# Performance work log

Measured on AMD Instinct MI355X. Metric: run time of the kernel, lower is better.

Reference implementation:

```python
import jax, jax.numpy as jnp
import numpy as np

N_FZ, N_KEZ, N_TINT, N_ALPHA = 60, 20, 30, 200
NORB, NTIMES = 2000, 1000


def setup_inputs() -> dict:
    key = jax.random.key(0)
    k1, k2, k3, k4 = jax.random.split(key, 4)
    # log-spaced coordinate axes (as built in __init__ from fZs / alphas)
    log_fZs = jnp.linspace(-11.0, -9.0, N_FZ, dtype=jnp.float32)
    log_alphas = jnp.linspace(-2.0, 0.0, N_ALPHA, dtype=jnp.float32)
    alphas = 10.0 ** log_alphas
    kEZs = jnp.linspace(0.5, 10.0, N_KEZ, dtype=jnp.float32)  # sorted for searchsorted
    # grid already in stored layout (n_fZ, n_kEZ, n_tint, n_alpha)
    grid = 20.0 + 5.0 * jax.random.uniform(k1, (N_FZ, N_KEZ, N_TINT, N_ALPHA), dtype=jnp.float32)
    # angular separations, mostly inside [alphas[0], alphas[-1]] with some outside
    alpha = 10.0 ** jax.random.uniform(k2, (NORB, NTIMES), minval=-2.2, maxval=0.1, dtype=jnp.float32)
    dMag = 20.0 + 5.0 * jax.random.uniform(k3, (NORB, NTIMES), dtype=jnp.float32)
    fZ_vals = 10.0 ** jax.random.uniform(k4, (NTIMES,), minval=-11.0, maxval=-9.0, dtype=jnp.float32)
    kEZ_val = jnp.asarray(3.0, dtype=jnp.float32)
    return dict(alpha=alpha, dMag=dMag, fZ_vals=fZ_vals, kEZ_val=kEZ_val,
                grid=grid, kEZs=kEZs, alphas=alphas, log_fZs=log_fZs, log_alphas=log_alphas)


def reference(alpha, dMag, fZ_vals, kEZ_val, grid, kEZs, alphas, log_fZs, log_alphas):
    """Faithful translation of dMag0Grid._pdet_alpha_dMag.

    alpha, dMag : (norb, ntimes); fZ_vals : (ntimes,); kEZ_val : scalar.
    grid : (n_fZ, n_kEZ, n_tint, n_alpha).  Returns pdet : (ntimes, n_tint).
    """
    n_fZ = grid.shape[0]
    n_alpha = grid.shape[-1]
    inv_log_fZ_step = 1.0 / (log_fZs[1] - log_fZs[0])
    inv_log_alpha_step = 1.0 / (log_alphas[1] - log_alphas[0])

    geom_mask = (alpha >= alphas[0]) & (alpha <= alphas[-1])  # (norb, ntimes)

    # log-binned fZ index, per time
    fZ_ind = (jnp.log10(fZ_vals) - log_fZs[0]) * inv_log_fZ_step
    fZ0 = jnp.clip(jnp.floor(fZ_ind).astype(jnp.int32) + 1, 0, n_fZ - 2)  # (ntimes,)

    # log-binned alpha index, per (orbit, time)
    a_ind = (jnp.log10(alpha) - log_alphas[0]) * inv_log_alpha_step
    a0 = jnp.clip(a_ind.astype(jnp.int32), 0, n_alpha - 1)  # (norb, ntimes)
    dalpha = (a_ind - a0).astype(grid.dtype)

    kEZ_ind = jnp.searchsorted(kEZs, kEZ_val, side='right') - 1  # scalar

    # dynamic_slice clamps start so the size-2 window stays in bounds
    a0s = jnp.minimum(a0, n_alpha - 2)
    fZb = jnp.broadcast_to(fZ0[None, :], a0.shape)  # (norb, ntimes)

    sub = grid[:, kEZ_ind]          # (n_fZ, n_tint, n_alpha)
    g0 = sub[fZb, :, a0s]           # (norb, ntimes, n_tint) gather
    g1 = sub[fZb, :, a0s + 1]
    dim = g0 + dalpha[..., None] * (g1 - g0)  # linear interp in log-alpha

    det_mask = geom_mask[..., None] & jnp.signbit(dMag[..., None] - dim)
    pdet = det_mask.mean(axis=0)    # (ntimes, n_tint)
    return pdet
```

## Files before the change

kernel.cpp:

```cpp
#include <hip/hip_runtime.h>
#include <math.h>

#define N_FZ    60
#define N_KEZ   20
#define N_TINT  30
#define N_ALPHA 200
#define NORB    2000
#define NTIMES  1000
#define BLOCK   1024
#define PAIR_LD 34
#define N_ROWS  199

__global__ __launch_bounds__(256) void prep_kernel(
    const float* __restrict__ alpha,
    const float* __restrict__ dMag,
    const float* __restrict__ alphas,
    const float* __restrict__ log_alphas,
    float2* __restrict__ xd)
{
    __shared__ float2 tile[32][33];

    const float la0    = log_alphas[0];
    const float inv_la = 1.0f / (log_alphas[1] - la0);
    const float alo    = alphas[0];
    const float ahi    = alphas[N_ALPHA - 1];

    const int t0 = blockIdx.x * 32;
    const int o0 = blockIdx.y * 32;
    const int tx = threadIdx.x, ty = threadIdx.y;

    #pragma unroll
    for (int r = 0; r < 4; ++r) {
        int orb = o0 + ty + 8 * r;
        int t   = t0 + tx;
        float2 v = make_float2(0.0f, __builtin_inff());
        if (orb < NORB && t < NTIMES) {
            float a  = alpha[(size_t)orb * NTIMES + t];
            float dm = dMag [(size_t)orb * NTIMES + t];
            bool geom = (a >= alo) && (a <= ahi);
            float x = (log10f(a) - la0) * inv_la;
            float xc = fminf(fmaxf(x, 0.0f), 198.9999f);
            v = make_float2(xc, geom ? dm : __builtin_inff());
        }
        tile[ty + 8 * r][tx] = v;
    }
    __syncthreads();
    #pragma unroll
    for (int r = 0; r < 4; ++r) {
        int tt  = ty + 8 * r;
        int t   = t0 + tt;
        int orb = o0 + tx;
        if (orb < NORB && t < NTIMES)
            xd[(size_t)t * NORB + orb] = tile[tx][tt];
    }
}

__global__ __launch_bounds__(BLOCK) void pdet6_kernel(
    const float2* __restrict__ xd,
    const float* __restrict__ fZ_vals,
    const float* __restrict__ kEZ_val,
    const float* __restrict__ grid,
    const float* __restrict__ kEZs,
    const float* __restrict__ log_fZs,
    float* __restrict__ out)
{
    __shared__ __align__(16) float2 gsT[N_ROWS * PAIR_LD];
    __shared__ int wsum[16][N_TINT];

    const int t   = blockIdx.x;
    const int tid = threadIdx.x;

    const float lf0    = log_fZs[0];
    const float lfstep = log_fZs[1] - lf0;
    double fZ_ind = (log10((double)fZ_vals[t]) - (double)lf0) * (1.0 / (double)lfstep);
    int fZ0 = (int)floor(fZ_ind) + 1;
    fZ0 = min(max(fZ0, 0), N_FZ - 2);

    const float kv = kEZ_val[0];
    int kidx = -1;
    #pragma unroll
    for (int i = 0; i < N_KEZ; ++i) kidx += (kEZs[i] <= kv) ? 1 : 0;
    if (kidx < 0) kidx += N_KEZ;

    const float* src = grid + ((size_t)fZ0 * N_KEZ + kidx) * (N_TINT * N_ALPHA);
    for (int m = tid; m < N_TINT * 256; m += BLOCK) {
        int k = m >> 8;
        int a = m & 255;
        if (a < N_ROWS) {
            const float* p = src + (size_t)k * N_ALPHA + a;
            float g0 = p[0];
            float g1 = p[1];
            gsT[a * PAIR_LD + k] = make_float2(g0, g1 - g0);
        }
    }
    __syncthreads();

    const int lane = tid & 63;
    const int w    = tid >> 6;
    const int s    = lane >> 4;
    const int h    = lane & 15;
    const int hh   = (h < 15) ? h : 14;

    const float2* row = xd + (size_t)t * NORB;

    int cnt_e = 0, cnt_o = 0;
    #pragma unroll 8
    for (int i = 0; i < 31; ++i) {
        int q = w + 16 * i;
        float2 v = row[4 * q + s];
        unsigned a0 = (unsigned)v.x;
        float dal = __builtin_amdgcn_fractf(v.x);
        float4 P = *reinterpret_cast<const float4*>(&gsT[a0 * PAIR_LD + 2 * hh]);
        cnt_e += (v.y < fmaf(dal, P.y, P.x)) ? 1 : 0;
        cnt_o += (v.y < fmaf(dal, P.w, P.z)) ? 1 : 0;
    }
    if (w < 4) {
        int q = 496 + w;
        float2 v = row[4 * q + s];
        unsigned a0 = (unsigned)v.x;
        float dal = __builtin_amdgcn_fractf(v.x);
        float4 P = *reinterpret_cast<const float4*>(&gsT[a0 * PAIR_LD + 2 * hh]);
        cnt_e += (v.y < fmaf(dal, P.y, P.x)) ? 1 : 0;
        cnt_o += (v.y < fmaf(dal, P.w, P.z)) ? 1 : 0;
    }

    cnt_e += __shfl_xor(cnt_e, 16, 64);
    cnt_e += __shfl_xor(cnt_e, 32, 64);
    cnt_o += __shfl_xor(cnt_o, 16, 64);
    cnt_o += __shfl_xor(cnt_o, 32, 64);
    if (lane < 15) {
        wsum[w][2 * lane]     = cnt_e;
        wsum[w][2 * lane + 1] = cnt_o;
    }
    __syncthreads();

    if (tid < N_TINT) {
        int tot = 0;
        #pragma unroll
        for (int w2 = 0; w2 < 16; ++w2) tot += wsum[w2][tid];
        out[(size_t)t * N_TINT + tid] = (float)tot * (1.0f / NORB);
    }
}

__global__ __launch_bounds__(256) void pdet_kernel(
    const float* __restrict__ alpha, const float* __restrict__ dMag,
    const float* __restrict__ fZ_vals, const float* __restrict__ kEZ_val,
    const float* __restrict__ grid, const float* __restrict__ kEZs,
    const float* __restrict__ alphas, const float* __restrict__ log_fZs,
    const float* __restrict__ log_alphas, float* __restrict__ out)
{
    __shared__ float2 pairs[N_TINT * (N_ALPHA + 1)];
    __shared__ int    wsum[4][N_TINT];

    const int t   = blockIdx.x;
    const int tid = threadIdx.x;

    const float la0    = log_alphas[0];
    const float inv_la = 1.0f / (log_alphas[1] - la0);
    const float alo    = alphas[0];
    const float ahi    = alphas[N_ALPHA - 1];

    const float lf0    = log_fZs[0];
    const float lfstep = log_fZs[1] - lf0;
    double fZ_ind = (log10((double)fZ_vals[t]) - (double)lf0) * (1.0 / (double)lfstep);
    int fZ0 = (int)floor(fZ_ind) + 1;
    fZ0 = min(max(fZ0, 0), N_FZ - 2);

    const float kv = kEZ_val[0];
    int kidx = -1;
    #pragma unroll
    for (int i = 0; i < N_KEZ; ++i) kidx += (kEZs[i] <= kv) ? 1 : 0;
    if (kidx < 0) kidx += N_KEZ;

    const float* src = grid + ((size_t)fZ0 * N_KEZ + kidx) * (N_TINT * N_ALPHA);
    for (int j = tid; j < N_TINT * N_ALPHA; j += 256) {
        int k = j / N_ALPHA;
        int a = j - k * N_ALPHA;
        float g0 = src[j];
        float g1 = (a < N_ALPHA - 1) ? src[j + 1] : g0;
        pairs[k * (N_ALPHA + 1) + a] = make_float2(g0, g1);
    }
    __syncthreads();

    int cnt[N_TINT];
    #pragma unroll
    for (int k = 0; k < N_TINT; ++k) cnt[k] = 0;

    for (int orb = tid; orb < NORB; orb += 256) {
        float a  = alpha[(size_t)orb * NTIMES + t];
        float dm = dMag [(size_t)orb * NTIMES + t];
        bool geom = (a >= alo) && (a <= ahi);
        float a_ind = (log10f(a) - la0) * inv_la;
        int a0 = (int)a_ind;
        a0 = min(max(a0, 0), N_ALPHA - 1);
        float dal = a_ind - (float)a0;
        int a0s = min(a0, N_ALPHA - 2);
        if (!geom) dm = __builtin_inff();

        #pragma unroll
        for (int k = 0; k < N_TINT; ++k) {
            float2 p = pairs[k * (N_ALPHA + 1) + a0s];
            float dim = p.x + dal * (p.y - p.x);
            cnt[k] += (dm < dim) ? 1 : 0;
        }
    }

    const int lane = tid & 63;
    const int wid  = tid >> 6;
    #pragma unroll
    for (int k = 0; k < N_TINT; ++k) {
        int c = cnt[k];
        c += __shfl_xor(c, 32, 64);
        c += __shfl_xor(c, 16, 64);
        c += __shfl_xor(c,  8, 64);
        c += __shfl_xor(c,  4, 64);
        c += __shfl_xor(c,  2, 64);
        c += __shfl_xor(c,  1, 64);
        if (lane == 0) wsum[wid][k] = c;
    }
    __syncthreads();

    if (tid < N_TINT) {
        int tot = wsum[0][tid] + wsum[1][tid] + wsum[2][tid] + wsum[3][tid];
        out[(size_t)t * N_TINT + tid] = (float)tot / (float)NORB;
    }
}

extern "C" void kernel_launch(void* const* d_in, const int* in_sizes, int n_in,
                              void* d_out, int out_size, void* d_ws, size_t ws_size,
                              hipStream_t stream) {
    const float* alpha      = (const float*)d_in[0];
    const float* dMag       = (const float*)d_in[1];
    const float* fZ_vals    = (const float*)d_in[2];
    const float* kEZ_val    = (const float*)d_in[3];
    const float* grid       = (const float*)d_in[4];
    const float* kEZs       = (const float*)d_in[5];
    const float* alphas     = (const float*)d_in[6];
    const float* log_fZs    = (const float*)d_in[7];
    const float* log_alphas = (const float*)d_in[8];
    float* out = (float*)d_out;

    const size_t need = (size_t)NTIMES * NORB * sizeof(float2);
    if (ws_size >= need) {
        dim3 gb((NTIMES + 31) / 32, (NORB + 31) / 32);
        dim3 tb(32, 8);
        prep_kernel<<<gb, tb, 0, stream>>>(alpha, dMag, alphas, log_alphas,
                                           (float2*)d_ws);
        pdet6_kernel<<<NTIMES, BLOCK, 0, stream>>>(
            (const float2*)d_ws, fZ_vals, kEZ_val, grid, kEZs, log_fZs, out);
    } else {
        pdet_kernel<<<NTIMES, 256, 0, stream>>>(
            alpha, dMag, fZ_vals, kEZ_val, grid, kEZs, alphas, log_fZs,
            log_alphas, out);
    }
}
```

Before: 119.9 us.

## Store interpolation table as fp16 pairs and process four t_int values per lane

The shared-memory table of (g0, g1-g0) pairs is packed as half2 instead of float2, which halves the table size. Each lane now reads a uint4 covering four integration-time entries and handles two orbit records per float4 load, so the work is split into 8 lanes per record instead of 16. This aims to cut LDS traffic and the number of instructions in the count loop. The cost is fp16 rounding of grid values around 20-25, which can flip detection comparisons close to the threshold and may drift from the reference.

```diff
diff --git a/kernel.cpp b/kernel.cpp
--- a/kernel.cpp
+++ b/kernel.cpp
@@ -1,4 +1,5 @@
 #include <hip/hip_runtime.h>
+#include <hip/hip_fp16.h>
 #include <math.h>
 
 #define N_FZ    60
@@ -8,7 +9,7 @@
 #define NORB    2000
 #define NTIMES  1000
 #define BLOCK   1024
-#define PAIR_LD 34
+#define ROW_U32 36
 #define N_ROWS  199
 
 __global__ __launch_bounds__(256) void prep_kernel(
@@ -55,7 +56,7 @@
     }
 }
 
-__global__ __launch_bounds__(BLOCK) void pdet6_kernel(
+__global__ __launch_bounds__(BLOCK) void pdet8_kernel(
     const float2* __restrict__ xd,
     const float* __restrict__ fZ_vals,
     const float* __restrict__ kEZ_val,
@@ -64,8 +65,8 @@
     const float* __restrict__ log_fZs,
     float* __restrict__ out)
 {
-    __shared__ __align__(16) float2 gsT[N_ROWS * PAIR_LD];
-    __shared__ int wsum[16][N_TINT];
+    __shared__ __align__(16) unsigned gsT[N_ROWS * ROW_U32];
+    __shared__ int wsum[16][32];
 
     const int t   = blockIdx.x;
     const int tid = threadIdx.x;
@@ -83,54 +84,75 @@
     if (kidx < 0) kidx += N_KEZ;
 
     const float* src = grid + ((size_t)fZ0 * N_KEZ + kidx) * (N_TINT * N_ALPHA);
-    for (int m = tid; m < N_TINT * 256; m += BLOCK) {
+    for (int m = tid; m < 32 * 256; m += BLOCK) {
         int k = m >> 8;
         int a = m & 255;
         if (a < N_ROWS) {
-            const float* p = src + (size_t)k * N_ALPHA + a;
-            float g0 = p[0];
-            float g1 = p[1];
-            gsT[a * PAIR_LD + k] = make_float2(g0, g1 - g0);
+            unsigned val = 0u;
+            if (k < N_TINT) {
+                const float* p = src + (size_t)k * N_ALPHA + a;
+                float g0 = p[0];
+                float g1 = p[1];
+                __half2 h2 = __halves2half2(__float2half(g0), __float2half(g1 - g0));
+                val = *reinterpret_cast<unsigned*>(&h2);
+            }
+            gsT[a * ROW_U32 + k] = val;
         }
     }
     __syncthreads();
 
     const int lane = tid & 63;
     const int w    = tid >> 6;
-    const int s    = lane >> 4;
-    const int h    = lane & 15;
-    const int hh   = (h < 15) ? h : 14;
-
-    const float2* row = xd + (size_t)t * NORB;
-
-    int cnt_e = 0, cnt_o = 0;
-    #pragma unroll 8
-    for (int i = 0; i < 31; ++i) {
-        int q = w + 16 * i;
-        float2 v = row[4 * q + s];
-        unsigned a0 = (unsigned)v.x;
-        float dal = __builtin_amdgcn_fractf(v.x);
-        float4 P = *reinterpret_cast<const float4*>(&gsT[a0 * PAIR_LD + 2 * hh]);
-        cnt_e += (v.y < fmaf(dal, P.y, P.x)) ? 1 : 0;
-        cnt_o += (v.y < fmaf(dal, P.w, P.z)) ? 1 : 0;
-    }
-    if (w < 4) {
-        int q = 496 + w;
-        float2 v = row[4 * q + s];
-        unsigned a0 = (unsigned)v.x;
-        float dal = __builtin_amdgcn_fractf(v.x);
-        float4 P = *reinterpret_cast<const float4*>(&gsT[a0 * PAIR_LD + 2 * hh]);
-        cnt_e += (v.y < fmaf(dal, P.y, P.x)) ? 1 : 0;
-        cnt_o += (v.y < fmaf(dal, P.w, P.z)) ? 1 : 0;
-    }
-
-    cnt_e += __shfl_xor(cnt_e, 16, 64);
-    cnt_e += __shfl_xor(cnt_e, 32, 64);
-    cnt_o += __shfl_xor(cnt_o, 16, 64);
-    cnt_o += __shfl_xor(cnt_o, 32, 64);
-    if (lane < 15) {
-        wsum[w][2 * lane]     = cnt_e;
-        wsum[w][2 * lane + 1] = cnt_o;
+    const int s    = lane >> 3;
+    const int h    = lane & 7;
+    const int hoff = 4 * h;
+
+    int c0 = 0, c1 = 0, c2 = 0, c3 = 0;
+
+    const float4* rp = reinterpret_cast<const float4*>(xd + (size_t)t * NORB)
+                     + 8 * w + s;
+
+    #define EVALREC(XC, DM)                                                      \
+    do {                                                                         \
+        unsigned a0_ = (unsigned)(XC);                                           \
+        float dal_ = __builtin_amdgcn_fractf(XC);                                \
+        uint4 U_ = *reinterpret_cast<const uint4*>(&gsT[a0_ * ROW_U32 + hoff]);  \
+        __half2 p0_ = *reinterpret_cast<const __half2*>(&U_.x);                  \
+        __half2 p1_ = *reinterpret_cast<const __half2*>(&U_.y);                  \
+        __half2 p2_ = *reinterpret_cast<const __half2*>(&U_.z);                  \
+        __half2 p3_ = *reinterpret_cast<const __half2*>(&U_.w);                  \
+        c0 += ((DM) < fmaf(dal_, __half2float(__high2half(p0_)),                 \
+                           __half2float(__low2half(p0_)))) ? 1 : 0;              \
+        c1 += ((DM) < fmaf(dal_, __half2float(__high2half(p1_)),                 \
+                           __half2float(__low2half(p1_)))) ? 1 : 0;              \
+        c2 += ((DM) < fmaf(dal_, __half2float(__high2half(p2_)),                 \
+                           __half2float(__low2half(p2_)))) ? 1 : 0;              \
+        c3 += ((DM) < fmaf(dal_, __half2float(__high2half(p3_)),                 \
+                           __half2float(__low2half(p3_)))) ? 1 : 0;              \
+    } while (0)
+
+    #pragma unroll 3
+    for (int j = 0; j < 7; ++j) {
+        float4 v = rp[128 * j];
+        EVALREC(v.x, v.y);
+        EVALREC(v.z, v.w);
+    }
+    if (w < 13) {
+        float4 v = rp[128 * 7];
+        EVALREC(v.x, v.y);
+        EVALREC(v.z, v.w);
+    }
+    #undef EVALREC
+
+    c0 += __shfl_xor(c0, 8, 64);  c0 += __shfl_xor(c0, 16, 64);  c0 += __shfl_xor(c0, 32, 64);
+    c1 += __shfl_xor(c1, 8, 64);  c1 += __shfl_xor(c1, 16, 64);  c1 += __shfl_xor(c1, 32, 64);
+    c2 += __shfl_xor(c2, 8, 64);  c2 += __shfl_xor(c2, 16, 64);  c2 += __shfl_xor(c2, 32, 64);
+    c3 += __shfl_xor(c3, 8, 64);  c3 += __shfl_xor(c3, 16, 64);  c3 += __shfl_xor(c3, 32, 64);
+    if (lane < 8) {
+        wsum[w][4 * lane + 0] = c0;
+        wsum[w][4 * lane + 1] = c1;
+        wsum[w][4 * lane + 2] = c2;
+        wsum[w][4 * lane + 3] = c3;
     }
     __syncthreads();
 
@@ -246,7 +268,7 @@
         dim3 tb(32, 8);
         prep_kernel<<<gb, tb, 0, stream>>>(alpha, dMag, alphas, log_alphas,
                                            (float2*)d_ws);
-        pdet6_kernel<<<NTIMES, BLOCK, 0, stream>>>(
+        pdet8_kernel<<<NTIMES, BLOCK, 0, stream>>>(
             (const float2*)d_ws, fZ_vals, kEZ_val, grid, kEZs, log_fZs, out);
     } else {
         pdet_kernel<<<NTIMES, 256, 0, stream>>>(
```

Measured after the change: 119.3 us. About the same (-0.5%).
